# Optimization experiments

Measured on AMD Instinct MI355X. Metric: run time of the kernel, lower is better.

Reference implementation:

```python
import jax, jax.numpy as jnp
import numpy as np

S, V = 64, 32          # input scalar / vector multiplicities (64x0e + 32x1o)
MID_S, MID_V = 96, 96  # irreps_mid = 64x0e+32x0e + 64x1o+32x1o
NB = 10                # number_of_basis (radial edge scalars)
N_NODES, N_EDGES = 50000, 400000


def _fctp_attr(xs, xv, attr, Ws, Wv):
    # FullyConnectedTensorProduct(x, node_attr='1x0e'): per-irrep-block linear
    # mixing scaled by the scalar attr, path weight 1/sqrt(fan_in).
    os = (xs @ Ws) * attr * (1.0 / np.sqrt(xs.shape[1]))
    ov = jnp.einsum('nui,uk->nki', xv, Wv) * attr[..., None] * (1.0 / np.sqrt(xv.shape[1]))
    return os, ov


def _conv(ns, nv, attr, src, dst, sh, esc,
          Wsc_s, Wsc_v, Wl1_s, Wl1_v, Wfc1, Wfc2, Wl2_s, Wl2_v, Wa):
    # GraphConvolutionWithNodeAttrs: gather -> weighted e3nn TP -> scatter-mean
    N, E = ns.shape[0], src.shape[0]
    # radial MLP (e3nn FullyConnectedNet, silu) -> per-edge tp weights (192)
    h = jax.nn.silu(esc @ Wfc1 * (1.0 / np.sqrt(esc.shape[1])))
    w = h @ Wfc2 * (1.0 / np.sqrt(h.shape[1]))
    w1, w2, w3, w4 = w[:, :64], w[:, 64:128], w[:, 128:160], w[:, 160:192]
    sc_s, sc_v = _fctp_attr(ns, nv, attr, Wsc_s, Wsc_v)   # self connection
    hs, hv = _fctp_attr(ns, nv, attr, Wl1_s, Wl1_v)       # lin1
    gs, gv = hs[src], hv[src]                              # gather by edge_src
    sh0, shv = sh[:, 0:1], sh[:, 1:4]                      # 1x0e, 1x1o edge sh
    # 'uvu' instructions: (0e x 0e -> 0e), (1o x 1o -> 0e), (0e x 1o -> 1o), (1o x 0e -> 1o)
    m_s = jnp.concatenate([
        gs * sh0 * w1,                                                     # [E,64]
        jnp.einsum('evi,ei->ev', gv, shv) * (1.0 / np.sqrt(3.0)) * w4],   # [E,32]
        axis=1)                                                            # [E,96]
    m_v = jnp.concatenate([
        gs[:, :, None] * shv[:, None, :] * w2[:, :, None],  # [E,64,3]
        gv * sh0[:, :, None] * w3[:, :, None]],              # [E,32,3]
        axis=1)                                              # [E,96,3]
    # scatter with reduce='mean' onto destination nodes
    deg = jnp.maximum(jax.ops.segment_sum(jnp.ones((E,), ns.dtype), dst, num_segments=N), 1.0)
    Ms = jax.ops.segment_sum(m_s, dst, num_segments=N) / deg[:, None]
    Mv = jax.ops.segment_sum(m_v, dst, num_segments=N) / deg[:, None, None]
    alpha = (Ms @ Wa) * (1.0 / np.sqrt(MID_S)) * attr      # [N,1] (output_mask==1)
    os, ov = _fctp_attr(Ms, Mv, attr, Wl2_s, Wl2_v)        # lin2
    return sc_s + alpha * os, sc_v + alpha[..., None] * ov


def _forward(node_s, node_v, node_attr, edge_src, edge_dst, edge_sh, edge_scalars, p1, p2):
    s, v = _conv(node_s, node_v, node_attr, edge_src, edge_dst, edge_sh, edge_scalars, *p1)
    # Gate: 64 scalars (silu) | 32 gates (sigmoid) gating 32x1o vectors
    gs = jax.nn.silu(s[:, :64])
    v = v * jax.nn.sigmoid(s[:, 64:96])[:, :, None]
    s2, v2 = _conv(gs, v, node_attr, edge_src, edge_dst, edge_sh, edge_scalars, *p2)
    return jnp.concatenate([s2, v2.reshape(v2.shape[0], -1)], axis=1)  # [N,160]


def setup_inputs():
    ks = jax.random.split(jax.random.key(0), 32)
    N, E = N_NODES, N_EDGES
    g = lambda i, shape: jax.random.normal(ks[i], shape, jnp.float32)
    inp = {'node_s': g(0, (N, S)),
           'node_v': g(1, (N, V, 3)),
           'node_attr': jnp.ones((N, 1), jnp.float32),
           'edge_src': jax.random.randint(ks[2], (E,), 0, N),
           'edge_dst': jax.random.randint(ks[3], (E,), 0, N),
           'edge_sh': g(4, (E, 4)),
           'edge_scalars': jax.random.uniform(ks[5], (E, NB), jnp.float32)}
    dims = {1: (96, 32), 2: (64, 32)}  # layer1 conv out feeds gate; layer2 is final conv
    i = 6
    for L in (1, 2):
        o_s, o_v = dims[L]
        for name, shape in [('sc_s', (S, o_s)), ('sc_v', (V, o_v)), ('lin1_s', (S, S)),
                            ('lin1_v', (V, V)), ('fc1', (NB, 64)), ('fc2', (64, 192)),
                            ('lin2_s', (MID_S, o_s)), ('lin2_v', (MID_V, o_v)), ('alpha', (MID_S, 1))]:
            inp['l%d_%s' % (L, name)] = g(i, shape)
            i += 1
    return inp


def reference(node_s, node_v, node_attr, edge_src, edge_dst, edge_sh, edge_scalars,
              l1_sc_s, l1_sc_v, l1_lin1_s, l1_lin1_v, l1_fc1, l1_fc2, l1_lin2_s, l1_lin2_v, l1_alpha,
              l2_sc_s, l2_sc_v, l2_lin1_s, l2_lin1_v, l2_fc1, l2_fc2, l2_lin2_s, l2_lin2_v, l2_alpha):
    p1 = (l1_sc_s, l1_sc_v, l1_lin1_s, l1_lin1_v, l1_fc1, l1_fc2, l1_lin2_s, l1_lin2_v, l1_alpha)
    p2 = (l2_sc_s, l2_sc_v, l2_lin1_s, l2_lin1_v, l2_fc1, l2_fc2, l2_lin2_s, l2_lin2_v, l2_alpha)
    return _forward(node_s, node_v, node_attr, edge_src, edge_dst, edge_sh, edge_scalars, p1, p2)
```

## Files before the change

kernel.cpp:

```cpp
#include <hip/hip_runtime.h>
#include <hip/hip_bf16.h>

#define INV_SQRT10 0.31622776601683794f
#define INV_SQRT64 0.125f
#define INV_SQRT32 0.17677669529663687f
#define INV_SQRT96 0.10206207261596575f
#define INV_SQRT3  0.5773502691896258f

typedef __attribute__((ext_vector_type(4))) float f32x4;
typedef __attribute__((ext_vector_type(8))) short bf16x8;

__device__ __forceinline__ unsigned short f2bf(float x) {
    union { float f; unsigned u; } v; v.f = x;
    unsigned r = v.u + 0x7FFF + ((v.u >> 16) & 1);
    return (unsigned short)(r >> 16);
}
__device__ __forceinline__ float bf2f(unsigned short u) {
    union { unsigned u; float f; } v; v.u = ((unsigned)u) << 16;
    return v.f;
}

__global__ __launch_bounds__(256) void k_prep_nodes(
    const float* __restrict__ ns, const float* __restrict__ nv,
    const int* __restrict__ dst,
    unsigned short* __restrict__ xsb, unsigned short* __restrict__ xvpb,
    int* __restrict__ cnt, int N, int E)
{
    const int gid = blockIdx.x * 256 + threadIdx.x, gs = gridDim.x * 256;
    for (int i = gid; i < N * 64; i += gs) xsb[i] = f2bf(ns[i]);
    for (int i = gid; i < N * 96; i += gs) {
        const int n = i / 96, rem = i - n * 96;
        const int ic = rem >> 5, u = rem & 31;
        xvpb[i] = f2bf(nv[(size_t)n * 96 + u * 3 + ic]);
    }
    for (int i = gid; i < E; i += gs) atomicAdd(&cnt[dst[i]], 1);
}

template <int OS>
__global__ __launch_bounds__(256) void k_prep_w(
    const float* __restrict__ Wl1s, const float* __restrict__ Wscs,
    const float* __restrict__ Wl1v, const float* __restrict__ Wscv,
    const float* __restrict__ Wfc2,
    const float* __restrict__ W2s, const float* __restrict__ W2v,
    const float* __restrict__ Wa,
    unsigned short* __restrict__ wsb, unsigned short* __restrict__ wvb,
    unsigned short* __restrict__ wfb,
    unsigned short* __restrict__ wob, unsigned short* __restrict__ wv2b)
{
    constexpr int NC1 = 64 + OS;
    constexpr int PC1 = ((OS + 16 + 15) / 16) * 16;
    const int gid = blockIdx.x * 256 + threadIdx.x, gs = gridDim.x * 256;
    for (int i = gid; i < NC1 * 64; i += gs) {
        const int c = i >> 6, k = i & 63;
        const float v = (c < 64) ? Wl1s[k * 64 + c] : Wscs[k * OS + (c - 64)];
        wsb[i] = f2bf(v);
    }
    for (int i = gid; i < 64 * 32; i += gs) {
        const int c = i >> 5, u = i & 31;
        const float v = (c < 32) ? Wl1v[u * 32 + c] : Wscv[u * 32 + (c - 32)];
        wvb[i] = f2bf(v);
    }
    for (int i = gid; i < 192 * 64; i += gs) {
        const int c = i >> 6, k = i & 63;
        wfb[i] = f2bf(Wfc2[k * 192 + c]);
    }
    for (int i = gid; i < PC1 * 96; i += gs) {
        const int c = i / 96, u = i - c * 96;
        float v = 0.f;
        if (c < OS) v = W2s[u * OS + c];
        else if (c == OS) v = Wa[u];
        wob[i] = f2bf(v);
    }
    for (int i = gid; i < 32 * 96; i += gs) {
        const int c = i / 96, u = i - c * 96;
        wv2b[i] = f2bf(W2v[u * 32 + c]);
    }
}

__global__ __launch_bounds__(256) void k_scan1(const int* __restrict__ cnt,
                                               int* __restrict__ partial, int N)
{
    __shared__ int lds[256];
    const int t = threadIdx.x, i = blockIdx.x * 256 + t;
    int v = (i < N) ? cnt[i] : 0;
    lds[t] = v;
    __syncthreads();
    for (int off = 128; off > 0; off >>= 1) {
        if (t < off) lds[t] += lds[t + off];
        __syncthreads();
    }
    if (t == 0) partial[blockIdx.x] = lds[0];
}

__global__ __launch_bounds__(1024) void k_scan2(int* __restrict__ partial, int NB)
{
    __shared__ int lds[1024];
    const int t = threadIdx.x;
    int v = (t < NB) ? partial[t] : 0;
    lds[t] = v;
    __syncthreads();
    for (int off = 1; off < 1024; off <<= 1) {
        int w = (t >= off) ? lds[t - off] : 0;
        __syncthreads();
        lds[t] += w;
        __syncthreads();
    }
    if (t < NB) partial[t] = lds[t] - v;
}

__global__ __launch_bounds__(256) void k_scan3(const int* __restrict__ cnt,
                                               const int* __restrict__ partial,
                                               int* __restrict__ base, int N)
{
    __shared__ int lds[256];
    const int t = threadIdx.x, i = blockIdx.x * 256 + t;
    int v = (i < N) ? cnt[i] : 0;
    lds[t] = v;
    __syncthreads();
    for (int off = 1; off < 256; off <<= 1) {
        int w = (t >= off) ? lds[t - off] : 0;
        __syncthreads();
        lds[t] += w;
        __syncthreads();
    }
    if (i < N) base[i] = partial[blockIdx.x] + lds[t] - v;
}

__global__ __launch_bounds__(256) void k_order(
    const int* __restrict__ dst, const int* __restrict__ base,
    int* __restrict__ cursor, int* __restrict__ order, int E)
{
    int i = blockIdx.x * 256 + threadIdx.x;
    if (i < E) {
        const int d = dst[i];
        order[base[d] + atomicAdd(&cursor[d], 1)] = i;
    }
}

__global__ __launch_bounds__(256) void k_gather(
    const int* __restrict__ order,
    const int* __restrict__ src, const float* __restrict__ sh,
    const float* __restrict__ esc,
    int* __restrict__ src_ord, float4* __restrict__ sh_ord,
    unsigned short* __restrict__ esc_ordb, int E)
{
    int pos = blockIdx.x * 256 + threadIdx.x;
    if (pos < E) {
        const int e = order[pos];
        src_ord[pos] = src[e];
        sh_ord[pos] = ((const float4*)sh)[e];
        const float* ep = esc + (size_t)e * 10;
        unsigned short* eo = esc_ordb + (size_t)pos * 10;
        #pragma unroll
        for (int q = 0; q < 10; q++) eo[q] = f2bf(ep[q]);
    }
}

template <int OS>
__global__ __launch_bounds__(256) void k_node_mfma(
    const unsigned short* __restrict__ xsb, const unsigned short* __restrict__ xvpb,
    const float* __restrict__ attr,
    const unsigned short* __restrict__ wsb, const unsigned short* __restrict__ wvb,
    unsigned short* __restrict__ hsb, unsigned short* __restrict__ hvbb,
    unsigned short* __restrict__ scs, unsigned short* __restrict__ scv, int N)
{
    constexpr int NC1 = 64 + OS;
    constexpr int CT1 = NC1 / 16;
    __shared__ float attr_l[64];
    const int tid = threadIdx.x;
    const int n0 = blockIdx.x * 64;
    if (tid < 64) attr_l[tid] = (n0 + tid < N) ? attr[n0 + tid] : 0.f;
    __syncthreads();
    const int wv = tid >> 6, lane = tid & 63;
    const int mrow = lane & 15, kg = lane >> 4;

    {
        const int rbase = wv * 16;
        const int r = rbase + mrow;
        const int rc = min(n0 + r, N - 1);
        const bf16x8 a0 = *(const bf16x8*)(xsb + (size_t)rc * 64 + kg * 8);
        const bf16x8 a1 = *(const bf16x8*)(xsb + (size_t)rc * 64 + 32 + kg * 8);
        f32x4 acc[CT1];
        #pragma unroll
        for (int t = 0; t < CT1; t++) acc[t] = (f32x4){0.f, 0.f, 0.f, 0.f};
        #pragma unroll
        for (int t = 0; t < CT1; t++) {
            const int c = t * 16 + mrow;
            const bf16x8 b0 = *(const bf16x8*)(wsb + c * 64 + kg * 8);
            const bf16x8 b1 = *(const bf16x8*)(wsb + c * 64 + 32 + kg * 8);
            acc[t] = __builtin_amdgcn_mfma_f32_16x16x32_bf16(a0, b0, acc[t], 0, 0, 0);
            acc[t] = __builtin_amdgcn_mfma_f32_16x16x32_bf16(a1, b1, acc[t], 0, 0, 0);
        }
        #pragma unroll
        for (int t = 0; t < CT1; t++) {
            const int c = t * 16 + mrow;
            #pragma unroll
            for (int rg = 0; rg < 4; rg++) {
                const int row = rbase + kg * 4 + rg;
                const int n = n0 + row;
                if (n < N) {
                    const float v = acc[t][rg] * INV_SQRT64 * attr_l[row];
                    if (c < 64) hsb[(size_t)n * 64 + c] = f2bf(v);
                    else        scs[(size_t)n * OS + (c - 64)] = f2bf(v);
                }
            }
        }
    }
    #pragma unroll
    for (int j = 0; j < 3; j++) {
        const int rbase = (wv * 3 + j) * 16;
        const int rv = rbase + mrow;
        const int ic = rv >> 6, nloc = rv & 63;
        const int nc = min(n0 + nloc, N - 1);
        const bf16x8 a = *(const bf16x8*)(xvpb + (size_t)nc * 96 + ic * 32 + kg * 8);
        f32x4 acc2[4];
        #pragma unroll
        for (int t = 0; t < 4; t++) acc2[t] = (f32x4){0.f, 0.f, 0.f, 0.f};
        #pragma unroll
        for (int t = 0; t < 4; t++) {
            const int c = t * 16 + mrow;
            const bf16x8 b = *(const bf16x8*)(wvb + c * 32 + kg * 8);
            acc2[t] = __builtin_amdgcn_mfma_f32_16x16x32_bf16(a, b, acc2[t], 0, 0, 0);
        }
        #pragma unroll
        for (int t = 0; t < 4; t++) {
            const int c = t * 16 + mrow;
            #pragma unroll
            for (int rg = 0; rg < 4; rg++) {
                const int rv2 = rbase + kg * 4 + rg;
                const int ic2 = rv2 >> 6, nl = rv2 & 63;
                const int n = n0 + nl;
                if (n < N) {
                    const float v = acc2[t][rg] * INV_SQRT32 * attr_l[nl];
                    if (c < 32) hvbb[(size_t)n * 96 + ic2 * 32 + c] = f2bf(v);
                    else        scv[(size_t)n * 96 + ic2 * 32 + (c - 32)] = f2bf(v);
                }
            }
        }
    }
}

__global__ __launch_bounds__(256) void k_edge_mlp(
    const unsigned short* __restrict__ esc_ordb, const int* __restrict__ base,
    const float* __restrict__ Wfc1, const unsigned short* __restrict__ wfb,
    unsigned* __restrict__ wbuf12, unsigned short* __restrict__ wbufB,
    int n0, int n1, int N, int E, int cap)
{
    __shared__ float esc_l[640];
    __shared__ float w1_l[640];
    __shared__ __align__(16) char hb[64 * 64 * 2];
    const int tid = threadIdx.x;
    const int lo = (n0 == 0) ? 0 : base[n0];
    const int hi = (n1 >= N) ? E : base[n1];
    const int p0 = lo + blockIdx.x * 64;
    if (p0 >= hi) return;

    for (int i = tid; i < 640; i += 256) w1_l[i] = Wfc1[i];
    {
        const size_t emax = (size_t)E * 10 - 1;
        for (int i = tid; i < 640; i += 256) {
            size_t idx = (size_t)p0 * 10 + i;
            esc_l[i] = bf2f(esc_ordb[idx > emax ? emax : idx]);
        }
    }
    __syncthreads();
    {
        const int r = tid >> 2, c0 = (tid & 3) << 4;
        float hval[16];
        #pragma unroll
        for (int c = 0; c < 16; c++) {
            float acc = 0.f;
            #pragma unroll
            for (int q = 0; q < 10; q++) acc += esc_l[r * 10 + q] * w1_l[q * 64 + c0 + c];
            acc *= INV_SQRT10;
            hval[c] = acc / (1.f + __expf(-acc));
        }
        unsigned pk[8];
        #pragma unroll
        for (int j = 0; j < 8; j++)
            pk[j] = (unsigned)f2bf(hval[2 * j]) | ((unsigned)f2bf(hval[2 * j + 1]) << 16);
        const int swz = (r & 7) << 4;
        const int b0 = (r << 7) + (c0 << 1);
        *(uint4*)(hb + (b0 ^ swz)) = make_uint4(pk[0], pk[1], pk[2], pk[3]);
        *(uint4*)(hb + ((b0 + 16) ^ swz)) = make_uint4(pk[4], pk[5], pk[6], pk[7]);
    }
    __syncthreads();
    const int wv = tid >> 6, lane = tid & 63;
    const int mrow = lane & 15, kgrp = lane >> 4;
    f32x4 acc[12];
    #pragma unroll
    for (int t = 0; t < 12; t++) acc[t] = (f32x4){0.f, 0.f, 0.f, 0.f};
    #pragma unroll
    for (int kc = 0; kc < 2; kc++) {
        const int r = wv * 16 + mrow;
        const int abyte = ((r << 7) + (kc << 6) + (kgrp << 4)) ^ ((r & 7) << 4);
        const bf16x8 afrag = *(const bf16x8*)(hb + abyte);
        #pragma unroll
        for (int t = 0; t < 12; t++) {
            const int c = t * 16 + mrow;
            const bf16x8 bfrag = *(const bf16x8*)(wfb + c * 64 + kc * 32 + kgrp * 8);
            acc[t] = __builtin_amdgcn_mfma_f32_16x16x32_bf16(afrag, bfrag, acc[t], 0, 0, 0);
        }
    }
    #pragma unroll
    for (int rg = 0; rg < 4; rg++) {
        const int rloc = wv * 16 + kgrp * 4 + rg;
        const int pos = p0 + rloc;
        if (pos < hi && (pos - lo) < cap) {
            uint4 pk12;
            pk12.x = (unsigned)f2bf(acc[0][rg] * INV_SQRT64) | ((unsigned)f2bf(acc[4][rg] * INV_SQRT64) << 16);
            pk12.y = (unsigned)f2bf(acc[1][rg] * INV_SQRT64) | ((unsigned)f2bf(acc[5][rg] * INV_SQRT64) << 16);
            pk12.z = (unsigned)f2bf(acc[2][rg] * INV_SQRT64) | ((unsigned)f2bf(acc[6][rg] * INV_SQRT64) << 16);
            pk12.w = (unsigned)f2bf(acc[3][rg] * INV_SQRT64) | ((unsigned)f2bf(acc[7][rg] * INV_SQRT64) << 16);
            ushort4 pkB;
            pkB.x = f2bf(acc[8][rg] * INV_SQRT64);
            pkB.y = f2bf(acc[9][rg] * INV_SQRT64);
            pkB.z = f2bf(acc[10][rg] * INV_SQRT64);
            pkB.w = f2bf(acc[11][rg] * INV_SQRT64);
            *(uint4*)(wbuf12 + (size_t)(pos - lo) * 64 + mrow * 4) = pk12;
            *(ushort4*)(wbufB + (size_t)(pos - lo) * 64 + mrow * 4) = pkB;
        }
    }
}

__global__ __launch_bounds__(256) void k_agg(
    const unsigned short* __restrict__ hsb, const unsigned short* __restrict__ hvbb,
    const int* __restrict__ src_ord, const float4* __restrict__ sh_ord,
    const int* __restrict__ base, const int* __restrict__ cnt,
    const unsigned* __restrict__ wbuf12, const unsigned short* __restrict__ wbufB,
    unsigned short* __restrict__ Msb, unsigned short* __restrict__ Mvb,
    int n0, int n1, int N, int E)
{
    const int wave = threadIdx.x >> 6, lane = threadIdx.x & 63;
    const int n = n0 + blockIdx.x * 4 + wave;
    if (n >= n1) return;
    const int lo = (n0 == 0) ? 0 : base[n0];
    const int cidx = (lane & 15) * 4 + (lane >> 4);

    float aS = 0.f, aSB = 0.f;
    float aV0 = 0.f, aV1 = 0.f, aV2 = 0.f;
    float aB0 = 0.f, aB1 = 0.f, aB2 = 0.f;
    const int b0 = base[n];
    const int c_ = cnt[n];
    const size_t wb = (size_t)(b0 - lo) * 64;
    int s_nx = (c_ > 0) ? src_ord[b0] : 0;
    for (int j = 0; j < c_; ++j) {
        const int s = s_nx;
        if (j + 1 < c_) s_nx = src_ord[b0 + j + 1];
        const unsigned p12 = wbuf12[wb + (size_t)j * 64 + cidx];
        const float w1 = bf2f((unsigned short)(p12 & 0xFFFF));
        const float w2 = bf2f((unsigned short)(p12 >> 16));
        const float wB = bf2f(wbufB[wb + (size_t)j * 64 + cidx]);
        const float gs = bf2f(hsb[(size_t)s * 64 + lane]);
        float gv0 = 0.f, gv1 = 0.f, gv2 = 0.f;
        if (lane < 32) {
            gv0 = bf2f(hvbb[(size_t)s * 96 + lane]);
            gv1 = bf2f(hvbb[(size_t)s * 96 + 32 + lane]);
            gv2 = bf2f(hvbb[(size_t)s * 96 + 64 + lane]);
        }
        const float4 s4 = sh_ord[b0 + j];
        const float gvdot = gv0 * s4.y + gv1 * s4.z + gv2 * s4.w;
        const float gvd = __shfl(gvdot, lane & 31);
        aS  += gs * s4.x * w1;
        aSB += gvd * INV_SQRT3 * wB;
        aV0 += gs * s4.y * w2;
        aV1 += gs * s4.z * w2;
        aV2 += gs * s4.w * w2;
        aB0 += gv0 * s4.x * wB;
        aB1 += gv1 * s4.x * wB;
        aB2 += gv2 * s4.x * wB;
    }
    const float invd = 1.f / (float)max(c_, 1);
    unsigned short* msp = Msb + (size_t)n * 96;
    unsigned short* mvp = Mvb + (size_t)n * 3 * 96;
    msp[lane] = f2bf(aS * invd);
    if (lane >= 32) msp[64 + (lane - 32)] = f2bf(aSB * invd);
    mvp[0 * 96 + lane] = f2bf(aV0 * invd);
    mvp[1 * 96 + lane] = f2bf(aV1 * invd);
    mvp[2 * 96 + lane] = f2bf(aV2 * invd);
    if (lane < 32) {
        mvp[0 * 96 + 64 + lane] = f2bf(aB0 * invd);
        mvp[1 * 96 + 64 + lane] = f2bf(aB1 * invd);
        mvp[2 * 96 + 64 + lane] = f2bf(aB2 * invd);
    }
}

template <int OS, bool FINAL>
__global__ __launch_bounds__(256) void k_node_out(
    const unsigned short* __restrict__ Msb, const unsigned short* __restrict__ Mvb,
    const float* __restrict__ attr,
    const unsigned short* __restrict__ scs, const unsigned short* __restrict__ scv,
    const unsigned short* __restrict__ wob, const unsigned short* __restrict__ wv2b,
    float* __restrict__ outF,
    unsigned short* __restrict__ outSb, unsigned short* __restrict__ outVb, int N)
{
    constexpr int CT1 = (OS + 16 + 15) / 16;
    constexpr int TA = OS / 16;
    __shared__ float attr_l[64];
    __shared__ float alpha_l[64];
    __shared__ float gate_l[64][32];
    const int tid = threadIdx.x;
    const int n0 = blockIdx.x * 64;
    if (tid < 64) attr_l[tid] = (n0 + tid < N) ? attr[n0 + tid] : 0.f;
    __syncthreads();
    const int wv = tid >> 6, lane = tid & 63;
    const int mrow = lane & 15, kg = lane >> 4;

    const int rbase = wv * 16;
    const int rc = min(n0 + rbase + mrow, N - 1);
    f32x4 acc[CT1];
    #pragma unroll
    for (int t = 0; t < CT1; t++) acc[t] = (f32x4){0.f, 0.f, 0.f, 0.f};
    #pragma unroll
    for (int kc = 0; kc < 3; kc++) {
        const bf16x8 a = *(const bf16x8*)(Msb + (size_t)rc * 96 + kc * 32 + kg * 8);
        #pragma unroll
        for (int t = 0; t < CT1; t++) {
            const bf16x8 b = *(const bf16x8*)(wob + (size_t)(t * 16 + mrow) * 96 + kc * 32 + kg * 8);
            acc[t] = __builtin_amdgcn_mfma_f32_16x16x32_bf16(a, b, acc[t], 0, 0, 0);
        }
    }
    if (mrow == 0) {
        #pragma unroll
        for (int rg = 0; rg < 4; rg++) {
            const int row = rbase + kg * 4 + rg;
            alpha_l[row] = acc[TA][rg] * INV_SQRT96 * attr_l[row];
        }
    }
    __syncthreads();
    #pragma unroll
    for (int t = 0; t < CT1; t++) {
        const int c = t * 16 + mrow;
        if (c < OS) {
            #pragma unroll
            for (int rg = 0; rg < 4; rg++) {
                const int row = rbase + kg * 4 + rg;
                const int n = n0 + row;
                if (n < N) {
                    const float os = acc[t][rg] * INV_SQRT96 * attr_l[row];
                    const float s = bf2f(scs[(size_t)n * OS + c]) + alpha_l[row] * os;
                    if (FINAL) {
                        outF[(size_t)n * 160 + c] = s;
                    } else {
                        if (c < 64) outSb[(size_t)n * 64 + c] = f2bf(s / (1.f + __expf(-s)));
                        else        gate_l[row][c - 64] = 1.f / (1.f + __expf(-s));
                    }
                }
            }
        }
    }
    __syncthreads();
    #pragma unroll
    for (int j = 0; j < 3; j++) {
        const int rb2 = (wv * 3 + j) * 16;
        const int rv = rb2 + mrow;
        const int nl = rv / 3, ii = rv - nl * 3;
        const int nc2 = min(n0 + nl, N - 1);
        f32x4 acc2[2];
        acc2[0] = (f32x4){0.f, 0.f, 0.f, 0.f};
        acc2[1] = (f32x4){0.f, 0.f, 0.f, 0.f};
        #pragma unroll
        for (int kc = 0; kc < 3; kc++) {
            const bf16x8 a = *(const bf16x8*)(Mvb + ((size_t)nc2 * 3 + ii) * 96 + kc * 32 + kg * 8);
            #pragma unroll
            for (int t = 0; t < 2; t++) {
                const bf16x8 b = *(const bf16x8*)(wv2b + (size_t)(t * 16 + mrow) * 96 + kc * 32 + kg * 8);
                acc2[t] = __builtin_amdgcn_mfma_f32_16x16x32_bf16(a, b, acc2[t], 0, 0, 0);
            }
        }
        #pragma unroll
        for (int t = 0; t < 2; t++) {
            const int k = t * 16 + mrow;
            #pragma unroll
            for (int rg = 0; rg < 4; rg++) {
                const int rv2 = rb2 + kg * 4 + rg;
                const int nl2 = rv2 / 3, i2 = rv2 - nl2 * 3;
                const int n = n0 + nl2;
                if (n < N) {
                    const float ov = acc2[t][rg] * INV_SQRT96 * attr_l[nl2];
                    const float v = bf2f(scv[(size_t)n * 96 + i2 * 32 + k]) + alpha_l[nl2] * ov;
                    if (FINAL) outF[(size_t)n * 160 + 64 + k * 3 + i2] = v;
                    else       outVb[(size_t)n * 96 + i2 * 32 + k] = f2bf(v * gate_l[nl2][k]);
                }
            }
        }
    }
}

extern "C" void kernel_launch(void* const* d_in, const int* in_sizes, int n_in,
                              void* d_out, int out_size, void* d_ws, size_t ws_size,
                              hipStream_t stream)
{
    const float* node_s = (const float*)d_in[0];
    const float* node_v = (const float*)d_in[1];
    const float* attr   = (const float*)d_in[2];
    const int*   esrc   = (const int*)d_in[3];
    const int*   edst   = (const int*)d_in[4];
    const float* esh    = (const float*)d_in[5];
    const float* esc    = (const float*)d_in[6];
    const float* W[18];
    for (int i = 0; i < 18; i++) W[i] = (const float*)d_in[7 + i];

    const int N = in_sizes[0] / 64;
    const int E = in_sizes[3];
    const int NB = (N + 255) / 256;

    char* p = (char*)d_ws;
    unsigned short* xsb  = (unsigned short*)p; p += (size_t)N * 64 * 2;
    unsigned short* xvpb = (unsigned short*)p; p += (size_t)N * 96 * 2;
    unsigned short* hsb  = (unsigned short*)p; p += (size_t)N * 64 * 2;
    unsigned short* hvbb = (unsigned short*)p; p += (size_t)N * 96 * 2;
    unsigned short* Msb  = (unsigned short*)p; p += (size_t)N * 96 * 2;
    unsigned short* Mvb  = (unsigned short*)p; p += (size_t)N * 288 * 2;
    unsigned short* scs  = (unsigned short*)p; p += (size_t)N * 96 * 2;
    unsigned short* scv  = (unsigned short*)p; p += (size_t)N * 96 * 2;
    unsigned short* wsb1 = (unsigned short*)p; p += 160 * 64 * 2;
    unsigned short* wsb2 = (unsigned short*)p; p += 128 * 64 * 2;
    unsigned short* wvb1 = (unsigned short*)p; p += 64 * 32 * 2;
    unsigned short* wvb2 = (unsigned short*)p; p += 64 * 32 * 2;
    unsigned short* wfb1 = (unsigned short*)p; p += 192 * 64 * 2;
    unsigned short* wfb2 = (unsigned short*)p; p += 192 * 64 * 2;
    unsigned short* wob1 = (unsigned short*)p; p += 112 * 96 * 2;
    unsigned short* wob2 = (unsigned short*)p; p += 80 * 96 * 2;
    unsigned short* wv2b1 = (unsigned short*)p; p += 32 * 96 * 2;
    unsigned short* wv2b2 = (unsigned short*)p; p += 32 * 96 * 2;
    int* cnt    = (int*)p; p += (size_t)N * 4;
    int* cursor = (int*)p; p += (size_t)N * 4;
    int* basei  = (int*)p; p += (size_t)N * 4;
    int* partial = (int*)p; p += (size_t)NB * 4;
    p = (char*)(((size_t)p + 255) & ~(size_t)255);
    int* order   = (int*)p; p += (size_t)E * 4;
    int* src_ord = (int*)p; p += (size_t)E * 4;
    p = (char*)(((size_t)p + 15) & ~(size_t)15);
    float4* sh_ord = (float4*)p; p += (size_t)E * 16;
    unsigned short* esc_ordb = (unsigned short*)p; p += (size_t)E * 20;
    p = (char*)(((size_t)p + 255) & ~(size_t)255);
    const size_t used_fixed = (size_t)(p - (char*)d_ws);

    int NQ = 4;
    size_t cap = 0;
    {
        const int cands[3] = {1, 2, 4};
        for (int ci = 0; ci < 3; ci++) {
            const int c = cands[ci];
            size_t cc = (c == 1) ? (size_t)E : ((size_t)E / c) * 9 / 8 + 256;
            if (used_fixed + cc * 384 <= ws_size) { NQ = c; cap = cc; break; }
        }
        if (cap == 0) { NQ = 4; cap = ((size_t)E / 4) * 9 / 8 + 256; }
    }
    unsigned* wbuf12      = (unsigned*)p;       p += cap * 256;
    unsigned short* wbufB = (unsigned short*)p; p += cap * 128;

    const int nb  = (N + 63) / 64;
    const int ebk = (E + 255) / 256;
    const int Q   = (N + NQ - 1) / NQ;
    const int qb  = (Q + 3) / 4;
    const int emb = (int)((cap + 63) / 64);

    hipMemsetAsync(cnt, 0, (size_t)2 * N * sizeof(int), stream);
    k_prep_nodes<<<2048, 256, 0, stream>>>(node_s, node_v, edst, xsb, xvpb, cnt, N, E);
    k_prep_w<96><<<32, 256, 0, stream>>>(W[2], W[0], W[3], W[1], W[5], W[6], W[7], W[8],
                                         wsb1, wvb1, wfb1, wob1, wv2b1);
    k_prep_w<64><<<32, 256, 0, stream>>>(W[11], W[9], W[12], W[10], W[14], W[15], W[16], W[17],
                                         wsb2, wvb2, wfb2, wob2, wv2b2);
    k_scan1<<<NB, 256, 0, stream>>>(cnt, partial, N);
    k_scan2<<<1, 1024, 0, stream>>>(partial, NB);
    k_scan3<<<NB, 256, 0, stream>>>(cnt, partial, basei, N);
    k_order<<<ebk, 256, 0, stream>>>(edst, basei, cursor, order, E);
    k_gather<<<ebk, 256, 0, stream>>>(order, esrc, esh, esc,
                                      src_ord, sh_ord, esc_ordb, E);

    k_node_mfma<96><<<nb, 256, 0, stream>>>(xsb, xvpb, attr, wsb1, wvb1,
                                            hsb, hvbb, scs, scv, N);
    for (int q = 0; q < NQ; q++) {
        const int n0 = q * Q, n1 = min(N, (q + 1) * Q);
        if (n0 >= n1) break;
        k_edge_mlp<<<emb, 256, 0, stream>>>(esc_ordb, basei, W[4], wfb1,
                                            wbuf12, wbufB, n0, n1, N, E, (int)cap);
        k_agg<<<qb, 256, 0, stream>>>(hsb, hvbb, src_ord, sh_ord, basei, cnt,
                                      wbuf12, wbufB, Msb, Mvb, n0, n1, N, E);
    }
    k_node_out<96, false><<<nb, 256, 0, stream>>>(Msb, Mvb, attr, scs, scv,
                                                  wob1, wv2b1,
                                                  nullptr, xsb, xvpb, N);
    k_node_mfma<64><<<nb, 256, 0, stream>>>(xsb, xvpb, attr, wsb2, wvb2,
                                            hsb, hvbb, scs, scv, N);
    for (int q = 0; q < NQ; q++) {
        const int n0 = q * Q, n1 = min(N, (q + 1) * Q);
        if (n0 >= n1) break;
        k_edge_mlp<<<emb, 256, 0, stream>>>(esc_ordb, basei, W[13], wfb2,
                                            wbuf12, wbufB, n0, n1, N, E, (int)cap);
        k_agg<<<qb, 256, 0, stream>>>(hsb, hvbb, src_ord, sh_ord, basei, cnt,
                                      wbuf12, wbufB, Msb, Mvb, n0, n1, N, E);
    }
    k_node_out<64, true><<<nb, 256, 0, stream>>>(Msb, Mvb, attr, scs, scv,
                                                 wob2, wv2b2,
                                                 (float*)d_out, nullptr, nullptr, N);
}
```

Baseline: 545.6 us.

## Software-pipeline edge gather loop, stage MLP weights in LDS, use builtin bf16 convert

The per-node gather loop is software-pipelined so each iteration issues loads for the next edge (and the source index two ahead) before accumulating the current edge, hiding gather latency. The edge-MLP kernel now stages the fc2 weight matrix in swizzled shared memory instead of reading B fragments from global, and loads edge scalars straight into registers. The float-to-bf16 conversion now uses the HIP builtin cast. Costs are more registers in the gather kernel and extra LDS plus a per-block weight copy in the MLP kernel, which may lower occupancy.

```diff
diff --git a/kernel.cpp b/kernel.cpp
--- a/kernel.cpp
+++ b/kernel.cpp
@@ -11,9 +11,7 @@
 typedef __attribute__((ext_vector_type(8))) short bf16x8;
 
 __device__ __forceinline__ unsigned short f2bf(float x) {
-    union { float f; unsigned u; } v; v.f = x;
-    unsigned r = v.u + 0x7FFF + ((v.u >> 16) & 1);
-    return (unsigned short)(r >> 16);
+    return __builtin_bit_cast(unsigned short, (__hip_bfloat16)x);
 }
 __device__ __forceinline__ float bf2f(unsigned short u) {
     union { unsigned u; float f; } v; v.u = ((unsigned)u) << 16;
@@ -246,9 +244,9 @@
     unsigned* __restrict__ wbuf12, unsigned short* __restrict__ wbufB,
     int n0, int n1, int N, int E, int cap)
 {
-    __shared__ float esc_l[640];
     __shared__ float w1_l[640];
     __shared__ __align__(16) char hb[64 * 64 * 2];
+    __shared__ __align__(16) char wf_l[192 * 64 * 2];
     const int tid = threadIdx.x;
     const int lo = (n0 == 0) ? 0 : base[n0];
     const int hi = (n1 >= N) ? E : base[n1];
@@ -256,22 +254,31 @@
     if (p0 >= hi) return;
 
     for (int i = tid; i < 640; i += 256) w1_l[i] = Wfc1[i];
+    for (int i = tid; i < 1536; i += 256) {
+        const int c = i >> 3, k16 = i & 7;
+        const uint4 v = *(const uint4*)(wfb + c * 64 + k16 * 8);
+        *(uint4*)(wf_l + (((c << 7) + (k16 << 4)) ^ ((c & 7) << 4))) = v;
+    }
+    const int r = tid >> 2, c0 = (tid & 3) << 4;
+    float ev[10];
     {
-        const size_t emax = (size_t)E * 10 - 1;
-        for (int i = tid; i < 640; i += 256) {
-            size_t idx = (size_t)p0 * 10 + i;
-            esc_l[i] = bf2f(esc_ordb[idx > emax ? emax : idx]);
+        const int rc = min(p0 + r, E - 1);
+        const unsigned* ep = (const unsigned*)(esc_ordb + (size_t)rc * 10);
+        #pragma unroll
+        for (int q = 0; q < 5; q++) {
+            const unsigned u = ep[q];
+            ev[2 * q]     = bf2f((unsigned short)(u & 0xFFFF));
+            ev[2 * q + 1] = bf2f((unsigned short)(u >> 16));
         }
     }
     __syncthreads();
     {
-        const int r = tid >> 2, c0 = (tid & 3) << 4;
         float hval[16];
         #pragma unroll
         for (int c = 0; c < 16; c++) {
             float acc = 0.f;
             #pragma unroll
-            for (int q = 0; q < 10; q++) acc += esc_l[r * 10 + q] * w1_l[q * 64 + c0 + c];
+            for (int q = 0; q < 10; q++) acc += ev[q] * w1_l[q * 64 + c0 + c];
             acc *= INV_SQRT10;
             hval[c] = acc / (1.f + __expf(-acc));
         }
@@ -292,13 +299,14 @@
     for (int t = 0; t < 12; t++) acc[t] = (f32x4){0.f, 0.f, 0.f, 0.f};
     #pragma unroll
     for (int kc = 0; kc < 2; kc++) {
-        const int r = wv * 16 + mrow;
-        const int abyte = ((r << 7) + (kc << 6) + (kgrp << 4)) ^ ((r & 7) << 4);
+        const int rr = wv * 16 + mrow;
+        const int abyte = ((rr << 7) + (kc << 6) + (kgrp << 4)) ^ ((rr & 7) << 4);
         const bf16x8 afrag = *(const bf16x8*)(hb + abyte);
         #pragma unroll
         for (int t = 0; t < 12; t++) {
             const int c = t * 16 + mrow;
-            const bf16x8 bfrag = *(const bf16x8*)(wfb + c * 64 + kc * 32 + kgrp * 8);
+            const int bbyte = ((c << 7) + (kc << 6) + (kgrp << 4)) ^ ((c & 7) << 4);
+            const bf16x8 bfrag = *(const bf16x8*)(wf_l + bbyte);
             acc[t] = __builtin_amdgcn_mfma_f32_16x16x32_bf16(afrag, bfrag, acc[t], 0, 0, 0);
         }
     }
@@ -343,32 +351,57 @@
     const int b0 = base[n];
     const int c_ = cnt[n];
     const size_t wb = (size_t)(b0 - lo) * 64;
-    int s_nx = (c_ > 0) ? src_ord[b0] : 0;
+
+    unsigned p12A = 0; float wBA = 0.f, gsA = 0.f;
+    float gv0A = 0.f, gv1A = 0.f, gv2A = 0.f;
+    float4 s4A = make_float4(0.f, 0.f, 0.f, 0.f);
+    int s2 = 0;
+    if (c_ > 0) {
+        const int s1 = src_ord[b0];
+        s2 = (c_ > 1) ? src_ord[b0 + 1] : 0;
+        p12A = wbuf12[wb + cidx];
+        wBA = bf2f(wbufB[wb + cidx]);
+        gsA = bf2f(hsb[(size_t)s1 * 64 + lane]);
+        if (lane < 32) {
+            gv0A = bf2f(hvbb[(size_t)s1 * 96 + lane]);
+            gv1A = bf2f(hvbb[(size_t)s1 * 96 + 32 + lane]);
+            gv2A = bf2f(hvbb[(size_t)s1 * 96 + 64 + lane]);
+        }
+        s4A = sh_ord[b0];
+    }
     for (int j = 0; j < c_; ++j) {
-        const int s = s_nx;
-        if (j + 1 < c_) s_nx = src_ord[b0 + j + 1];
-        const unsigned p12 = wbuf12[wb + (size_t)j * 64 + cidx];
-        const float w1 = bf2f((unsigned short)(p12 & 0xFFFF));
-        const float w2 = bf2f((unsigned short)(p12 >> 16));
-        const float wB = bf2f(wbufB[wb + (size_t)j * 64 + cidx]);
-        const float gs = bf2f(hsb[(size_t)s * 64 + lane]);
-        float gv0 = 0.f, gv1 = 0.f, gv2 = 0.f;
-        if (lane < 32) {
-            gv0 = bf2f(hvbb[(size_t)s * 96 + lane]);
-            gv1 = bf2f(hvbb[(size_t)s * 96 + 32 + lane]);
-            gv2 = bf2f(hvbb[(size_t)s * 96 + 64 + lane]);
-        }
-        const float4 s4 = sh_ord[b0 + j];
-        const float gvdot = gv0 * s4.y + gv1 * s4.z + gv2 * s4.w;
-        const float gvd = __shfl(gvdot, lane & 31);
-        aS  += gs * s4.x * w1;
-        aSB += gvd * INV_SQRT3 * wB;
-        aV0 += gs * s4.y * w2;
-        aV1 += gs * s4.z * w2;
-        aV2 += gs * s4.w * w2;
-        aB0 += gv0 * s4.x * wB;
-        aB1 += gv1 * s4.x * wB;
-        aB2 += gv2 * s4.x * wB;
+        unsigned p12B = 0; float wBB = 0.f, gsB = 0.f;
+        float gv0B = 0.f, gv1B = 0.f, gv2B = 0.f;
+        float4 s4B = make_float4(0.f, 0.f, 0.f, 0.f);
+        if (j + 1 < c_) {
+            p12B = wbuf12[wb + (size_t)(j + 1) * 64 + cidx];
+            wBB = bf2f(wbufB[wb + (size_t)(j + 1) * 64 + cidx]);
+            gsB = bf2f(hsb[(size_t)s2 * 64 + lane]);
+            if (lane < 32) {
+                gv0B = bf2f(hvbb[(size_t)s2 * 96 + lane]);
+                gv1B = bf2f(hvbb[(size_t)s2 * 96 + 32 + lane]);
+                gv2B = bf2f(hvbb[(size_t)s2 * 96 + 64 + lane]);
+            }
+            s4B = sh_ord[b0 + j + 1];
+        }
+        const int s2n = (j + 2 < c_) ? src_ord[b0 + j + 2] : 0;
+        {
+            const float w1 = bf2f((unsigned short)(p12A & 0xFFFF));
+            const float w2 = bf2f((unsigned short)(p12A >> 16));
+            const float gvdot = gv0A * s4A.y + gv1A * s4A.z + gv2A * s4A.w;
+            const float gvd = __shfl(gvdot, lane & 31);
+            aS  += gsA * s4A.x * w1;
+            aSB += gvd * INV_SQRT3 * wBA;
+            aV0 += gsA * s4A.y * w2;
+            aV1 += gsA * s4A.z * w2;
+            aV2 += gsA * s4A.w * w2;
+            aB0 += gv0A * s4A.x * wBA;
+            aB1 += gv1A * s4A.x * wBA;
+            aB2 += gv2A * s4A.x * wBA;
+        }
+        p12A = p12B; wBA = wBB; gsA = gsB;
+        gv0A = gv0B; gv1A = gv1B; gv2A = gv2B;
+        s4A = s4B; s2 = s2n;
     }
     const float invd = 1.f / (float)max(c_, 1);
     unsigned short* msp = Msb + (size_t)n * 96;
```

After: 465.6 us. 14.7% less time.
